# Kernel tuning notes

Hardware: AMD Instinct MI355X
Metric: run time of the kernel (lower is better)

## Reference

```python
import jax, jax.numpy as jnp
import numpy as np

N = 100000      # nodes
E = 1600000     # edges
IN = 128        # in_channels
HEADS = 4
HID = 32        # hidden_channels (per-head dim)
HD = HEADS * HID  # 128, concat output dim
OUT = 2         # out_channels


def setup_inputs() -> dict:
    key = jax.random.key(0)
    ks = jax.random.split(key, 18)

    def lin(kw, kb, fan_in, fan_out):
        lim = 1.0 / np.sqrt(fan_in)
        W = jax.random.uniform(kw, (fan_in, fan_out), jnp.float32, -lim, lim)
        b = jax.random.uniform(kb, (fan_out,), jnp.float32, -lim, lim)
        return W, b

    x = jax.random.normal(ks[0], (N, IN), jnp.float32)
    edge_index = jax.random.randint(ks[1], (2, E), 0, N, jnp.int32)

    Wq, bq = lin(ks[2], ks[3], IN, HD)   # lin_query
    Wk, bk = lin(ks[4], ks[5], IN, HD)   # lin_key
    Wv, bv = lin(ks[6], ks[7], IN, HD)   # lin_value
    Ws, bs = lin(ks[8], ks[9], IN, HD)   # lin_skip (root weight)
    W1, b1 = lin(ks[10], ks[11], HD, 6 * HEADS)  # readout Linear(128, 24)
    W2, b2 = lin(ks[12], ks[13], 6 * HEADS, 8)   # readout Linear(24, 8)
    W3, b3 = lin(ks[14], ks[15], 8, OUT)         # readout Linear(8, 2)

    return {"x": x, "edge_index": edge_index,
            "Wq": Wq, "bq": bq, "Wk": Wk, "bk": bk, "Wv": Wv, "bv": bv,
            "Ws": Ws, "bs": bs, "W1": W1, "b1": b1, "W2": W2, "b2": b2,
            "W3": W3, "b3": b3}


def _tanhshrink(z):
    return z - jnp.tanh(z)


def reference(x, edge_index, Wq, bq, Wk, bk, Wv, bv, Ws, bs,
              W1, b1, W2, b2, W3, b3):
    n = x.shape[0]
    src, dst = edge_index[0], edge_index[1]  # messages flow src -> dst

    # TransformerConv: per-node Q/K/V projections, reshaped to heads
    q = (x @ Wq + bq).reshape(n, HEADS, HID)
    k = (x @ Wk + bk).reshape(n, HEADS, HID)
    v = (x @ Wv + bv).reshape(n, HEADS, HID)

    # per-edge gather + attention logits [E, H]
    scale = 1.0 / np.float32(np.sqrt(HID))
    scores = jnp.einsum('ehd,ehd->eh', q[dst], k[src]) * scale

    # segment softmax over incoming edges of each dst node (numerically stable)
    m = jax.ops.segment_max(scores, dst, num_segments=n)
    m = jnp.where(jnp.isfinite(m), m, 0.0)  # guard isolated nodes
    e = jnp.exp(scores - m[dst])
    denom = jax.ops.segment_sum(e, dst, num_segments=n)
    alpha = e / denom[dst]  # [E, H]

    # weighted scatter-aggregate of values, concat heads, add root skip
    agg = jax.ops.segment_sum(alpha[:, :, None] * v[src], dst,
                              num_segments=n).reshape(n, HD)
    h = jnp.tanh(agg + x @ Ws + bs)  # bn() in source is an identity reshape

    # readout MLP (Dropout p=0.01 omitted: eval mode)
    h1 = _tanhshrink(h @ W1 + b1)
    h2 = _tanhshrink(h1 @ W2 + b2)
    return h2 @ W3 + b3
```

## Files before the change

### kernel.cpp

```cpp
#include <hip/hip_runtime.h>
#include <hip/hip_bf16.h>
#include <hip/hip_fp16.h>
#include <math.h>

#define NN 100000
#define EE 1600000
#define HD_ 128
#define PART 8
#define RNG 12500
#define SCATB 1024
#define CAP 64
#define PROJ_GRID 768
#define NTILES (NN / 16)

typedef float f32x4 __attribute__((ext_vector_type(4)));
typedef _Float16 f16x8 __attribute__((ext_vector_type(8)));
typedef _Float16 f16x2 __attribute__((ext_vector_type(2)));
typedef float accf4 __attribute__((ext_vector_type(4)));

__device__ __forceinline__ float fast_tanh(float z) {
    float az = fabsf(z);
    float e = __expf(-2.f * az);
    float t = (1.f - e) / (1.f + e);
    return copysignf(t, z);
}

struct alignas(16) h8 { __half2 h[4]; };
struct alignas(8)  h4 { __half2 a, b; };

__global__ __launch_bounds__(256) void scatter_wt(
    const int* __restrict__ ei, int* __restrict__ cnt, int* __restrict__ ssrc,
    const float* __restrict__ Wq, const float* __restrict__ Wk,
    const float* __restrict__ Wv, const float* __restrict__ Ws,
    __half* __restrict__ Wt)
{
    if (blockIdx.x < 32) {
        const int t = blockIdx.x * 256 + threadIdx.x;
        const int lane = t & 63;
        const int kt = (t >> 6) & 3;
        const int ct = (t >> 8) & 7;
        const int mat = t >> 11;
        const float* Wm = (mat == 0) ? Wq : (mat == 1) ? Wk
                        : (mat == 2) ? Wv : Ws;
        const int col = ct * 16 + (lane & 15);
        const int k0 = kt * 32 + (lane >> 4) * 8;
        h8 hh;
#pragma unroll
        for (int j = 0; j < 4; ++j) {
            hh.h[j] = __floats2half2_rn(Wm[(size_t)(k0 + 2 * j) * 128 + col],
                                        Wm[(size_t)(k0 + 2 * j + 1) * 128 + col]);
        }
        *reinterpret_cast<h8*>(Wt + (size_t)t * 8) = hh;
    }

    const int g = blockIdx.x & (PART - 1);
    const int bg = blockIdx.x >> 3;
    const int lo = g * RNG;
    const int hi = lo + RNG;
    const int idx = bg * 256 + threadIdx.x;
    for (int q = idx; q < EE / 4; q += (SCATB / PART) * 256) {
        const int e = q * 4;
        const int4 d4 = *reinterpret_cast<const int4*>(ei + EE + e);
        const int dd[4] = {d4.x, d4.y, d4.z, d4.w};
#pragma unroll
        for (int j = 0; j < 4; ++j) {
            const int d = dd[j];
            if (d >= lo && d < hi) {
                int pos = atomicAdd(&cnt[d], 1);
                if (pos < CAP) ssrc[(d << 6) | pos] = ei[e + j];
            }
        }
    }
}

__global__ __launch_bounds__(256) void proj_mfma(
    const float* __restrict__ x, const __half* __restrict__ Wt,
    const float* __restrict__ bq, const float* __restrict__ bk,
    const float* __restrict__ bv, const float* __restrict__ bs,
    __half* __restrict__ Qh, __half* __restrict__ Sh, __half* __restrict__ KV)
{
    __shared__ __half xs[16][136];
    __shared__ __half ys[16][520];
    const int tid = threadIdx.x;
    const int w = tid >> 6;
    const int lane = tid & 63;

    f16x8 wf[32];
    {
        const __half* wbase = Wt + (size_t)w * 16384;
#pragma unroll
        for (int i = 0; i < 32; ++i)
            wf[i] = *reinterpret_cast<const f16x8*>(
                wbase + (size_t)(i * 64 + lane) * 8);
    }

    const float* bm = (w == 0) ? bq : (w == 1) ? bk : (w == 2) ? bv : bs;
    const float sc = (w == 0) ? 0.17677669529663687f : 1.f;

    const int srow = tid & 15;
    const int sk0 = (tid >> 4) * 8;

    int t = blockIdx.x;
    f32x4 ra, rb;
    if (t < NTILES) {
        const f32x4* xp = reinterpret_cast<const f32x4*>(
            x + (size_t)(t * 16 + srow) * 128 + sk0);
        ra = __builtin_nontemporal_load(xp);
        rb = __builtin_nontemporal_load(xp + 1);
    }

    for (; t < NTILES; t += PROJ_GRID) {
        const int n0 = t * 16;

        {
            h8 hh;
            hh.h[0] = __floats2half2_rn(ra.x, ra.y);
            hh.h[1] = __floats2half2_rn(ra.z, ra.w);
            hh.h[2] = __floats2half2_rn(rb.x, rb.y);
            hh.h[3] = __floats2half2_rn(rb.z, rb.w);
            *reinterpret_cast<h8*>(&xs[srow][sk0]) = hh;
        }
        __syncthreads();

        if (t + PROJ_GRID < NTILES) {
            const f32x4* xp = reinterpret_cast<const f32x4*>(
                x + (size_t)((t + PROJ_GRID) * 16 + srow) * 128 + sk0);
            ra = __builtin_nontemporal_load(xp);
            rb = __builtin_nontemporal_load(xp + 1);
        }

        f16x8 bx[4];
#pragma unroll
        for (int kt = 0; kt < 4; ++kt)
            bx[kt] = *reinterpret_cast<const f16x8*>(
                &xs[lane & 15][kt * 32 + (lane >> 4) * 8]);

#pragma unroll
        for (int ct = 0; ct < 8; ++ct) {
            accf4 acc = {0.f, 0.f, 0.f, 0.f};
#pragma unroll
            for (int kt = 0; kt < 4; ++kt)
                acc = __builtin_amdgcn_mfma_f32_16x16x32_f16(
                    wf[ct * 4 + kt], bx[kt], acc, 0, 0, 0);
            const float4 bb = *reinterpret_cast<const float4*>(
                bm + ct * 16 + ((lane >> 4) << 2));
            h4 o;
            o.a = __floats2half2_rn((acc[0] + bb.x) * sc, (acc[1] + bb.y) * sc);
            o.b = __floats2half2_rn((acc[2] + bb.z) * sc, (acc[3] + bb.w) * sc);
            *reinterpret_cast<h4*>(
                &ys[lane & 15][w * 128 + ct * 16 + ((lane >> 4) << 2)]) = o;
        }
        __syncthreads();

        {
            const int node = tid >> 4;
            const int c8 = (tid & 15) * 8;
            h8 q = *reinterpret_cast<h8*>(&ys[node][c8]);
            h8 k = *reinterpret_cast<h8*>(&ys[node][128 + c8]);
            h8 v = *reinterpret_cast<h8*>(&ys[node][256 + c8]);
            h8 s = *reinterpret_cast<h8*>(&ys[node][384 + c8]);
            *reinterpret_cast<h8*>(Qh + (size_t)(n0 + node) * 128 + c8) = q;
            *reinterpret_cast<h8*>(KV + (size_t)(n0 + node) * 256 + c8) = k;
            *reinterpret_cast<h8*>(KV + (size_t)(n0 + node) * 256 + 128 + c8) = v;
            *reinterpret_cast<h8*>(Sh + (size_t)(n0 + node) * 128 + c8) = s;
        }
    }
}

__global__ __launch_bounds__(256) void attn_kernel(
    const __half* __restrict__ Qh, const __half* __restrict__ KV,
    const __half* __restrict__ Sh,
    const int* __restrict__ cnt, const int* __restrict__ ssrc,
    __half* __restrict__ hbuf)
{
    const int wid = threadIdx.x >> 6;
    const int lane = threadIdx.x & 63;
    const int node = blockIdx.x * 4 + wid;
    const int eg = lane >> 4;
    const int li = lane & 15;

    h8 qq = *reinterpret_cast<const h8*>(Qh + (size_t)node * 128 + li * 8);
    f16x2 qp[4];
#pragma unroll
    for (int j = 0; j < 4; ++j)
        qp[j] = *reinterpret_cast<const f16x2*>(&qq.h[j]);

    float a[8];
#pragma unroll
    for (int j = 0; j < 8; ++j) a[j] = 0.f;
    float l = 0.f;

    const int st = node << 6;
    int dg = cnt[node];
    if (dg > CAP) dg = CAP;

    for (int it = 0; it < dg; it += 16) {
        const __half* rows[4];
        bool val[4];
#pragma unroll
        for (int b = 0; b < 4; ++b) {
            const int e = it + b * 4 + eg;
            val[b] = e < dg;
            const int src = ssrc[st + (val[b] ? e : 0)];
            rows[b] = KV + (size_t)src * 256 + li * 8;
        }

        h8 kk[4], vv[4];
#pragma unroll
        for (int b = 0; b < 4; ++b) {
            kk[b] = *reinterpret_cast<const h8*>(rows[b]);
            vv[b] = *reinterpret_cast<const h8*>(rows[b] + 128);
        }

        float p[4];
#pragma unroll
        for (int b = 0; b < 4; ++b) {
            float s = 0.f;
#if __has_builtin(__builtin_amdgcn_fdot2)
#pragma unroll
            for (int j = 0; j < 4; ++j)
                s = __builtin_amdgcn_fdot2(
                        qp[j], *reinterpret_cast<const f16x2*>(&kk[b].h[j]),
                        s, false);
#else
#pragma unroll
            for (int j = 0; j < 4; ++j) {
                const float2 kf = __half22float2(kk[b].h[j]);
                const float2 qf = __half22float2(qq.h[j]);
                s = fmaf(qf.x, kf.x, s);
                s = fmaf(qf.y, kf.y, s);
            }
#endif
            p[b] = s;
        }

#pragma unroll
        for (int b = 0; b < 4; ++b) {
            p[b] += __shfl_xor(p[b], 1);
            p[b] += __shfl_xor(p[b], 2);
        }

        float w[4];
#pragma unroll
        for (int b = 0; b < 4; ++b) {
            w[b] = val[b] ? __expf(p[b]) : 0.f;
            l += w[b];
        }

#pragma unroll
        for (int b = 0; b < 4; ++b) {
#pragma unroll
            for (int j = 0; j < 4; ++j) {
                const float2 vf = __half22float2(vv[b].h[j]);
                a[2 * j]     = fmaf(w[b], vf.x, a[2 * j]);
                a[2 * j + 1] = fmaf(w[b], vf.y, a[2 * j + 1]);
            }
        }
    }

#pragma unroll
    for (int j = 0; j < 8; ++j) {
        a[j] += __shfl_xor(a[j], 16);
        a[j] += __shfl_xor(a[j], 32);
    }
    l += __shfl_xor(l, 16);
    l += __shfl_xor(l, 32);

    const float inv = (l > 0.f) ? 1.f / l : 0.f;

    if (eg == 0) {
        const h8 ss = *reinterpret_cast<const h8*>(Sh + (size_t)node * 128 + li * 8);
        h8 ho;
#pragma unroll
        for (int j = 0; j < 4; ++j) {
            const float2 sf = __half22float2(ss.h[j]);
            const float h0 = fast_tanh(a[2 * j] * inv + sf.x);
            const float h1 = fast_tanh(a[2 * j + 1] * inv + sf.y);
            ho.h[j] = __floats2half2_rn(h0, h1);
        }
        *reinterpret_cast<h8*>(hbuf + (size_t)node * 128 + li * 8) = ho;
    }
}

__global__ __launch_bounds__(256) void mlp_kernel(
    const __half* __restrict__ hbuf,
    const float* __restrict__ W1, const float* __restrict__ b1,
    const float* __restrict__ W2, const float* __restrict__ b2,
    const float* __restrict__ W3, const float* __restrict__ b3,
    float* __restrict__ out)
{
    __shared__ float W1s[128][24];
    __shared__ float W2s[24][8];
    __shared__ float W3s[8][2];
    __shared__ float b1s[24], b2s[8], b3s[2];

    const int tid = threadIdx.x;

    {
        const float4* src = reinterpret_cast<const float4*>(W1 + tid * 12);
        float4* dst = reinterpret_cast<float4*>(&W1s[0][0] + tid * 12);
        dst[0] = src[0];
        dst[1] = src[1];
        dst[2] = src[2];
        if (tid < 48)
            reinterpret_cast<float4*>(&W2s[0][0])[tid] =
                reinterpret_cast<const float4*>(W2)[tid];
        if (tid < 4)
            reinterpret_cast<float4*>(&W3s[0][0])[tid] =
                reinterpret_cast<const float4*>(W3)[tid];
        if (tid < 24) b1s[tid] = b1[tid];
        if (tid < 8)  b2s[tid] = b2[tid];
        if (tid < 2)  b3s[tid] = b3[tid];
    }
    __syncthreads();

    const int node = blockIdx.x * 256 + tid;
    if (node >= NN) return;

    float t24[24];
#pragma unroll
    for (int j = 0; j < 24; ++j) t24[j] = b1s[j];

    const h8* hrow = reinterpret_cast<const h8*>(hbuf + (size_t)node * 128);
#pragma unroll
    for (int c = 0; c < 16; ++c) {
        const h8 hh = hrow[c];
        float hf[8];
#pragma unroll
        for (int j = 0; j < 4; ++j) {
            const float2 f = __half22float2(hh.h[j]);
            hf[2 * j] = f.x;
            hf[2 * j + 1] = f.y;
        }
#pragma unroll
        for (int i = 0; i < 8; ++i) {
            const int kk = c * 8 + i;
#pragma unroll
            for (int j4 = 0; j4 < 6; ++j4) {
                const float4 w4 = *reinterpret_cast<const float4*>(&W1s[kk][j4 * 4]);
                t24[j4 * 4 + 0] = fmaf(hf[i], w4.x, t24[j4 * 4 + 0]);
                t24[j4 * 4 + 1] = fmaf(hf[i], w4.y, t24[j4 * 4 + 1]);
                t24[j4 * 4 + 2] = fmaf(hf[i], w4.z, t24[j4 * 4 + 2]);
                t24[j4 * 4 + 3] = fmaf(hf[i], w4.w, t24[j4 * 4 + 3]);
            }
        }
    }

    float u8[8];
#pragma unroll
    for (int j = 0; j < 8; ++j) u8[j] = b2s[j];
#pragma unroll
    for (int kk = 0; kk < 24; ++kk) {
        const float hv = t24[kk] - fast_tanh(t24[kk]);
#pragma unroll
        for (int j = 0; j < 8; ++j) u8[j] = fmaf(hv, W2s[kk][j], u8[j]);
    }

    float o0 = b3s[0], o1 = b3s[1];
#pragma unroll
    for (int kk = 0; kk < 8; ++kk) {
        const float hv = u8[kk] - fast_tanh(u8[kk]);
        o0 = fmaf(hv, W3s[kk][0], o0);
        o1 = fmaf(hv, W3s[kk][1], o1);
    }
    *reinterpret_cast<float2*>(out + (size_t)node * 2) = make_float2(o0, o1);
}

extern "C" void kernel_launch(void* const* d_in, const int* in_sizes, int n_in,
                              void* d_out, int out_size, void* d_ws, size_t ws_size,
                              hipStream_t stream)
{
    const float* x  = (const float*)d_in[0];
    const int*   ei = (const int*)d_in[1];
    const float* Wq = (const float*)d_in[2];
    const float* bq = (const float*)d_in[3];
    const float* Wk = (const float*)d_in[4];
    const float* bk = (const float*)d_in[5];
    const float* Wv = (const float*)d_in[6];
    const float* bv = (const float*)d_in[7];
    const float* Ws = (const float*)d_in[8];
    const float* bs = (const float*)d_in[9];
    const float* W1 = (const float*)d_in[10];
    const float* b1 = (const float*)d_in[11];
    const float* W2 = (const float*)d_in[12];
    const float* b2 = (const float*)d_in[13];
    const float* W3 = (const float*)d_in[14];
    const float* b3 = (const float*)d_in[15];
    float* out = (float*)d_out;

    __half* ws = (__half*)d_ws;
    __half* Qh = ws;
    __half* Sh = Qh + (size_t)NN * HD_;
    __half* KV = Sh + (size_t)NN * HD_;
    __half* hbuf = KV + (size_t)NN * 256;
    __half* Wt = hbuf + (size_t)NN * HD_;
    int* cnt  = (int*)(Wt + 65536);
    int* ssrc = cnt + NN;

    (void)hipMemsetAsync(cnt, 0, NN * sizeof(int), stream);

    scatter_wt<<<SCATB, 256, 0, stream>>>(ei, cnt, ssrc, Wq, Wk, Wv, Ws, Wt);
    proj_mfma<<<PROJ_GRID, 256, 0, stream>>>(x, Wt, bq, bk, bv, bs, Qh, Sh, KV);
    attn_kernel<<<NN / 4, 256, 0, stream>>>(Qh, KV, Sh, cnt, ssrc, hbuf);
    mlp_kernel<<<(NN + 255) / 256, 256, 0, stream>>>(hbuf, W1, b1, W2, b2,
                                                     W3, b3, out);
}
```

Baseline: 257.2 us.

## Replace redundant partitioned edge scan with two-pass bucketed scatter via FIFOs

The edge scatter previously had each partition group scan the full dst array, reading edges eight times. It now first buckets edges per block into per-partition FIFO segments, using shared-memory counters. A second kernel then drains each partition's segments and performs the per-node atomic inserts. This removes repeated reads but adds an intermediate FIFO write/read and an extra launch, and it can silently drop edges if a bucket exceeds its fixed capacity.

Measured after the change: 261.0 us. Within noise of the previous version (+1.5%).

```diff
diff --git a/kernel.cpp b/kernel.cpp
--- a/kernel.cpp
+++ b/kernel.cpp
@@ -8,10 +8,13 @@
 #define HD_ 128
 #define PART 8
 #define RNG 12500
-#define SCATB 1024
 #define CAP 64
 #define PROJ_GRID 768
 #define NTILES (NN / 16)
+#define ABLK 500
+#define ACHUNK 3200
+#define SEGCAP 800
+#define BBLK 1024
 
 typedef float f32x4 __attribute__((ext_vector_type(4)));
 typedef _Float16 f16x8 __attribute__((ext_vector_type(8)));
@@ -28,14 +31,17 @@
 struct alignas(16) h8 { __half2 h[4]; };
 struct alignas(8)  h4 { __half2 a, b; };
 
-__global__ __launch_bounds__(256) void scatter_wt(
-    const int* __restrict__ ei, int* __restrict__ cnt, int* __restrict__ ssrc,
+__global__ __launch_bounds__(256) void partA_kernel(
+    const int* __restrict__ ei, int2* __restrict__ fifo,
+    int* __restrict__ cntAB,
     const float* __restrict__ Wq, const float* __restrict__ Wk,
     const float* __restrict__ Wv, const float* __restrict__ Ws,
     __half* __restrict__ Wt)
 {
+    const int tid = threadIdx.x;
+
     if (blockIdx.x < 32) {
-        const int t = blockIdx.x * 256 + threadIdx.x;
+        const int t = blockIdx.x * 256 + tid;
         const int lane = t & 63;
         const int kt = (t >> 6) & 3;
         const int ct = (t >> 8) & 7;
@@ -53,22 +59,46 @@
         *reinterpret_cast<h8*>(Wt + (size_t)t * 8) = hh;
     }
 
+    __shared__ int lcnt[PART];
+    if (tid < PART) lcnt[tid] = 0;
+    __syncthreads();
+
+    const int b = blockIdx.x;
+    const int base = b * ACHUNK;
+    for (int q = tid; q < ACHUNK / 4; q += 256) {
+        const int e = base + q * 4;
+        const int4 d4 = *reinterpret_cast<const int4*>(ei + EE + e);
+        const int4 s4 = *reinterpret_cast<const int4*>(ei + e);
+        const int dd[4] = {d4.x, d4.y, d4.z, d4.w};
+        const int ss[4] = {s4.x, s4.y, s4.z, s4.w};
+#pragma unroll
+        for (int j = 0; j < 4; ++j) {
+            const int d = dd[j];
+            const int g = d / RNG;
+            const int pos = atomicAdd(&lcnt[g], 1);
+            if (pos < SEGCAP)
+                fifo[(size_t)(b * PART + g) * SEGCAP + pos] = make_int2(ss[j], d);
+        }
+    }
+    __syncthreads();
+    if (tid < PART)
+        cntAB[b * PART + tid] = min(lcnt[tid], SEGCAP);
+}
+
+__global__ __launch_bounds__(256) void partB_kernel(
+    const int2* __restrict__ fifo, const int* __restrict__ cntAB,
+    int* __restrict__ cnt, int* __restrict__ ssrc)
+{
     const int g = blockIdx.x & (PART - 1);
     const int bg = blockIdx.x >> 3;
-    const int lo = g * RNG;
-    const int hi = lo + RNG;
-    const int idx = bg * 256 + threadIdx.x;
-    for (int q = idx; q < EE / 4; q += (SCATB / PART) * 256) {
-        const int e = q * 4;
-        const int4 d4 = *reinterpret_cast<const int4*>(ei + EE + e);
-        const int dd[4] = {d4.x, d4.y, d4.z, d4.w};
-#pragma unroll
-        for (int j = 0; j < 4; ++j) {
-            const int d = dd[j];
-            if (d >= lo && d < hi) {
-                int pos = atomicAdd(&cnt[d], 1);
-                if (pos < CAP) ssrc[(d << 6) | pos] = ei[e + j];
-            }
+    const int tid = threadIdx.x;
+    for (int s = bg; s < ABLK; s += BBLK / PART) {
+        const int n = cntAB[s * PART + g];
+        const int2* seg = fifo + (size_t)(s * PART + g) * SEGCAP;
+        for (int i = tid; i < n; i += 256) {
+            const int2 e = seg[i];
+            const int pos = atomicAdd(&cnt[e.y], 1);
+            if (pos < CAP) ssrc[(e.y << 6) | pos] = e.x;
         }
     }
 }
@@ -394,12 +424,16 @@
     __half* KV = Sh + (size_t)NN * HD_;
     __half* hbuf = KV + (size_t)NN * 256;
     __half* Wt = hbuf + (size_t)NN * HD_;
-    int* cnt  = (int*)(Wt + 65536);
-    int* ssrc = cnt + NN;
+    int* cnt   = (int*)(Wt + 65536);
+    int* ssrc  = cnt + NN;
+    int2* fifo = (int2*)(ssrc + (size_t)NN * CAP);
+    int* cntAB = (int*)(fifo + (size_t)ABLK * PART * SEGCAP);
 
     (void)hipMemsetAsync(cnt, 0, NN * sizeof(int), stream);
 
-    scatter_wt<<<SCATB, 256, 0, stream>>>(ei, cnt, ssrc, Wq, Wk, Wv, Ws, Wt);
+    partA_kernel<<<ABLK, 256, 0, stream>>>(ei, fifo, cntAB,
+                                           Wq, Wk, Wv, Ws, Wt);
+    partB_kernel<<<BBLK, 256, 0, stream>>>(fifo, cntAB, cnt, ssrc);
     proj_mfma<<<PROJ_GRID, 256, 0, stream>>>(x, Wt, bq, bk, bv, bs, Qh, Sh, KV);
     attn_kernel<<<NN / 4, 256, 0, stream>>>(Qh, KV, Sh, cnt, ssrc, hbuf);
     mlp_kernel<<<(NN + 255) / 256, 256, 0, stream>>>(hbuf, W1, b1, W2, b2,
```
